# Kernel optimization log

Measured on AMD Instinct MI355X. Metric: run time of the kernel, lower is better.

Reference implementation:

```python
import jax, jax.numpy as jnp
import numpy as np

N, NFEAT, NHID, NCLASS, NLAYERS = 8192, 512, 128, 40, 3
NEG = -9e15

def _sparse_adj(key, n, density=0.002):
    u = jax.random.uniform(key, (n, n), dtype=jnp.float32)
    return jnp.where(u < density, u / density, 0.0)

def setup_inputs() -> dict:
    key = jax.random.key(0)
    ks = jax.random.split(key, 12)
    return {
        "x": jax.random.normal(ks[0], (N, NFEAT), dtype=jnp.float32),
        "adj1": _sparse_adj(ks[1], N),
        "adj2": _sparse_adj(ks[2], N),
        "adj_att": _sparse_adj(ks[3], N),
        "fc1_w": jax.random.normal(ks[4], (NLAYERS, NHID, NFEAT), dtype=jnp.float32) * (1.0 / np.sqrt(NFEAT)),
        "fc1_b": jnp.zeros((NLAYERS, NHID), jnp.float32),
        "Q_w": jax.random.normal(ks[5], (NLAYERS - 1, NHID, NHID), dtype=jnp.float32) * (1.0 / np.sqrt(NHID)),
        "Q_b": jnp.zeros((NLAYERS - 1, NHID), jnp.float32),
        "K_w": jax.random.normal(ks[6], (NLAYERS - 1, NHID, NHID), dtype=jnp.float32) * (1.0 / np.sqrt(NHID)),
        "K_b": jnp.zeros((NLAYERS - 1, NHID), jnp.float32),
        "hop_select": jnp.ones((NLAYERS,), jnp.float32),
        "w": jnp.ones((NLAYERS - 1, 2), jnp.float32),
        "clf_w": jax.random.normal(ks[7], (NCLASS, NHID * NLAYERS), dtype=jnp.float32) * (1.0 / np.sqrt(NHID * NLAYERS)),
        "clf_b": jnp.zeros((NCLASS,), jnp.float32),
    }

def _l2_normalize(x, eps=1e-12):
    # F.normalize(x, p=2, dim=1)
    n = jnp.sqrt(jnp.sum(x * x, axis=1, keepdims=True))
    return x / jnp.maximum(n, eps)

def reference(x, adj1, adj2, adj_att, fc1_w, fc1_b, Q_w, Q_b, K_w, K_b,
              hop_select, w, clf_w, clf_b):
    adj_list = [None, adj1, adj2]
    mask = jax.nn.softmax(hop_select)  # hop selection weights, shape [nlayers]
    outs = []
    for i in range(NLAYERS):
        tmp = x @ fc1_w[i].T + fc1_b[i]  # [N, nhid]
        if adj_list[i] is not None:
            adj = adj_list[i]
            W_att = jax.nn.softmax(w[i - 1])  # [2]
            tmp_att = adj_att @ tmp           # [N, nhid]
            # GCN1: linear then propagate with adj_att (act='None')
            Q = adj_att @ (tmp_att @ Q_w[i - 1].T + Q_b[i - 1])
            K = adj_att @ (tmp_att @ K_w[i - 1].T + K_b[i - 1])
            scores = Q @ K.T                  # [N, N]
            scores = jnp.where(adj > 0, scores, NEG)
            attention = jax.nn.softmax(scores, axis=-1) * W_att[0] + adj * W_att[1]
            tmp = attention @ tmp             # [N, nhid]
        tmp = _l2_normalize(tmp)
        outs.append(mask[i] * tmp)
    final = jnp.concatenate(outs, axis=1)     # [N, nhid*nlayers]
    out = jax.nn.relu(final) @ clf_w.T + clf_b  # dropout is identity in eval
    return jax.nn.log_softmax(out, axis=1)
```

## Files before the change

kernel.cpp:

```cpp
#include <hip/hip_runtime.h>
#include <hip/hip_bf16.h>

#define NN     8192
#define NFEAT  512
#define NHID   128
#define NCLASS 40
#define NLAY   3
#define CAPA   128
#define FSZ    ((size_t)NN * NHID)

typedef float f32x4 __attribute__((ext_vector_type(4)));

__global__ __launch_bounds__(256, 4) void k_d1(
    const float* __restrict__ x, const float* __restrict__ fc1w, const float* __restrict__ fc1b,
    const float* __restrict__ adjA, const float* __restrict__ hop, const float* __restrict__ w,
    float* __restrict__ tmps, float* __restrict__ f_mask, float* __restrict__ f_watt,
    float* __restrict__ colsum, float* __restrict__ rowsumA,
    int* __restrict__ cntsA, int* __restrict__ colsA, float* __restrict__ valsA)
{
    __shared__ float smem[3200];
    const int bx = blockIdx.x, tid = threadIdx.x;

    if (bx < 384) {
        float* As = smem;
        float* Bs = smem + 1088;
        const int tx = tid & 15, ty = tid >> 4;
        const int bm = (bx & 127) * 64;
        const int layer = bx >> 7;
        const int bn = layer * 128;
        float acc[4][8] = {};

        const int rA = tid >> 2, cA = (tid & 3) * 4;
        for (int kt = 0; kt < NFEAT; kt += 16) {
            f32x4 va = *reinterpret_cast<const f32x4*>(&x[(size_t)(bm + rA) * NFEAT + kt + cA]);
            As[(cA + 0) * 68 + rA] = va[0];
            As[(cA + 1) * 68 + rA] = va[1];
            As[(cA + 2) * 68 + rA] = va[2];
            As[(cA + 3) * 68 + rA] = va[3];
            #pragma unroll
            for (int it = 0; it < 2; ++it) {
                int L = tid + it * 256;
                int r = L >> 2, c4 = (L & 3) * 4;
                f32x4 vb = *reinterpret_cast<const f32x4*>(&fc1w[(size_t)(bn + r) * NFEAT + kt + c4]);
                Bs[(c4 + 0) * 132 + r] = vb[0];
                Bs[(c4 + 1) * 132 + r] = vb[1];
                Bs[(c4 + 2) * 132 + r] = vb[2];
                Bs[(c4 + 3) * 132 + r] = vb[3];
            }
            __syncthreads();
            #pragma unroll
            for (int kk = 0; kk < 16; ++kk) {
                f32x4 ra  = *reinterpret_cast<const f32x4*>(&As[kk * 68 + ty * 4]);
                f32x4 rb0 = *reinterpret_cast<const f32x4*>(&Bs[kk * 132 + tx * 4]);
                f32x4 rb1 = *reinterpret_cast<const f32x4*>(&Bs[kk * 132 + tx * 4 + 64]);
                #pragma unroll
                for (int i = 0; i < 4; ++i) {
                    #pragma unroll
                    for (int j = 0; j < 4; ++j) {
                        acc[i][j]     = fmaf(ra[i], rb0[j], acc[i][j]);
                        acc[i][j + 4] = fmaf(ra[i], rb1[j], acc[i][j + 4]);
                    }
                }
            }
            __syncthreads();
        }
        const float* bofs = fc1b + bn;
        #pragma unroll
        for (int i = 0; i < 4; ++i) {
            int m = bm + ty * 4 + i;
            #pragma unroll
            for (int j = 0; j < 8; ++j) {
                int lc = (j < 4) ? (tx * 4 + j) : (64 + tx * 4 + (j - 4));
                tmps[(size_t)layer * FSZ + (size_t)m * NHID + lc] = acc[i][j] + bofs[lc];
            }
        }
    } else if (bx < 384 + NN) {
        const int row = bx - 384;
        int* s_lcnt = (int*)smem;
        float* s_lsum = smem + 1;
        if (tid == 0) { *s_lcnt = 0; *s_lsum = 0.f; }
        __syncthreads();
        const f32x4* arow = reinterpret_cast<const f32x4*>(adjA + (size_t)row * NN);
        int* rc = colsA + (size_t)row * CAPA;
        float* rv = valsA + (size_t)row * CAPA;

        f32x4 v[8];
        #pragma unroll
        for (int i = 0; i < 8; ++i) v[i] = arow[tid + (i << 8)];

        float ls = 0.f;
        #pragma unroll
        for (int i = 0; i < 8; ++i) {
            const int c4 = tid + (i << 8);
            #pragma unroll
            for (int k = 0; k < 4; ++k) {
                if (v[i][k] > 0.f) {
                    int p = atomicAdd(s_lcnt, 1);
                    if (p < CAPA) { rc[p] = c4 * 4 + k; rv[p] = v[i][k]; }
                    ls += v[i][k];
                }
            }
        }
        if (ls != 0.f) atomicAdd(s_lsum, ls);
        __syncthreads();
        if (tid == 0) {
            int n = *s_lcnt;
            cntsA[row] = n < CAPA ? n : CAPA;
            rowsumA[row] = *s_lsum;
        }
    } else {
        colsum[tid] = 0.f;
        if (tid == 0) {
            float m = fmaxf(fmaxf(hop[0], hop[1]), hop[2]);
            float e0 = expf(hop[0] - m), e1 = expf(hop[1] - m), e2 = expf(hop[2] - m);
            float s = e0 + e1 + e2;
            f_mask[0] = e0 / s; f_mask[1] = e1 / s; f_mask[2] = e2 / s;
            for (int l = 0; l < 2; ++l) {
                float a = w[2 * l], b = w[2 * l + 1];
                float mm = fmaxf(a, b);
                float ea = expf(a - mm), eb = expf(b - mm);
                float ss = ea + eb;
                f_watt[2 * l] = ea / ss; f_watt[2 * l + 1] = eb / ss;
            }
        }
    }
}

__global__ __launch_bounds__(256, 4) void k_d2(
    const int* __restrict__ cntsA, const int* __restrict__ colsA, const float* __restrict__ valsA,
    const float* __restrict__ tmps, float* __restrict__ tmp_att, float* __restrict__ colsum,
    const float* __restrict__ adj1,
    int* __restrict__ cnts12, int* __restrict__ cols12, float* __restrict__ vals12)
{
    __shared__ int sc[CAPA];
    __shared__ float sv[CAPA];
    __shared__ int s_lcnt;
    const int bx = blockIdx.x, t = threadIdx.x;

    if (bx < NN) {
        const int row = bx;
        const int n = cntsA[row];
        for (int p = t; p < n; p += 256) { sc[p] = colsA[(size_t)row * CAPA + p]; sv[p] = valsA[(size_t)row * CAPA + p]; }
        __syncthreads();
        const int h = t >> 7, col = t & 127;
        const float* X = tmps + (size_t)(h + 1) * FSZ;
        float a0 = 0.f, a1 = 0.f, a2 = 0.f, a3 = 0.f;
        int p = 0;
        for (; p + 4 <= n; p += 4) {
            a0 = fmaf(sv[p],     X[(size_t)sc[p]     * NHID + col], a0);
            a1 = fmaf(sv[p + 1], X[(size_t)sc[p + 1] * NHID + col], a1);
            a2 = fmaf(sv[p + 2], X[(size_t)sc[p + 2] * NHID + col], a2);
            a3 = fmaf(sv[p + 3], X[(size_t)sc[p + 3] * NHID + col], a3);
        }
        for (; p < n; ++p) a0 = fmaf(sv[p], X[(size_t)sc[p] * NHID + col], a0);
        tmp_att[(size_t)h * FSZ + (size_t)row * NHID + col] = (a0 + a1) + (a2 + a3);
    } else if (bx < NN + 64) {
        const int c = bx - NN;
        const int h = t >> 7, col = t & 127;
        const float* X = tmps + (size_t)(h + 1) * FSZ + (size_t)c * 128 * NHID;
        float a = 0.f;
        for (int r = 0; r < 128; ++r) a += X[(size_t)r * NHID + col];
        atomicAdd(&colsum[h * NHID + col], a);
    } else {
        const int row = bx - NN - 64;
        if (t == 0) s_lcnt = 0;
        __syncthreads();
        const f32x4* arow = reinterpret_cast<const f32x4*>(adj1 + (size_t)row * NN);
        int* rc = cols12 + (size_t)row * CAPA;
        float* rv = vals12 + (size_t)row * CAPA;

        f32x4 v[8];
        #pragma unroll
        for (int i = 0; i < 8; ++i) v[i] = arow[t + (i << 8)];

        #pragma unroll
        for (int i = 0; i < 8; ++i) {
            const int c4 = t + (i << 8);
            #pragma unroll
            for (int k = 0; k < 4; ++k) {
                if (v[i][k] > 0.f) {
                    int p = atomicAdd(&s_lcnt, 1);
                    if (p < CAPA) { rc[p] = c4 * 4 + k; rv[p] = v[i][k]; }
                }
            }
        }
        __syncthreads();
        if (t == 0) cnts12[row] = s_lcnt < CAPA ? s_lcnt : CAPA;
    }
}

__global__ __launch_bounds__(256, 4) void k_d3(
    const int* __restrict__ cntsA, const int* __restrict__ colsA, const float* __restrict__ valsA,
    const float* __restrict__ tmp_att, const float* __restrict__ Qw, const float* __restrict__ Kw,
    const float* __restrict__ Qb, const float* __restrict__ Kb,
    const float* __restrict__ rowsumA, float* __restrict__ QKm,
    const float* __restrict__ adj2,
    int* __restrict__ cnts12, int* __restrict__ cols12, float* __restrict__ vals12)
{
    __shared__ float AsT[8192];
    const int b = blockIdx.x, tid = threadIdx.x;

    if (b < 256) {
        const int bm = (b & 127) * 64, Lz = b >> 7;
        const float* X = tmp_att + (size_t)Lz * FSZ;
        {
            const int lrow = tid >> 2, coff = (tid & 3) * 32;
            const int row = bm + lrow;
            f32x4 acc[8] = {};
            const int n = cntsA[row];
            const int* rc = colsA + (size_t)row * CAPA;
            const float* rv = valsA + (size_t)row * CAPA;
            for (int p = 0; p < n; ++p) {
                int c = rc[p];
                float v = rv[p];
                const f32x4* src = reinterpret_cast<const f32x4*>(X + (size_t)c * NHID + coff);
                #pragma unroll
                for (int j = 0; j < 8; ++j) {
                    f32x4 s = src[j];
                    acc[j][0] = fmaf(v, s[0], acc[j][0]);
                    acc[j][1] = fmaf(v, s[1], acc[j][1]);
                    acc[j][2] = fmaf(v, s[2], acc[j][2]);
                    acc[j][3] = fmaf(v, s[3], acc[j][3]);
                }
            }
            #pragma unroll
            for (int j = 0; j < 8; ++j)
                #pragma unroll
                for (int q = 0; q < 4; ++q)
                    AsT[(coff + j * 4 + q) * 64 + lrow] = acc[j][q];
        }
        __syncthreads();

        const int tx = tid & 15, ty = tid >> 4;
        float rs[4];
        #pragma unroll
        for (int i = 0; i < 4; ++i) rs[i] = rowsumA[bm + ty * 4 + i];
        float* C = QKm + (size_t)Lz * NN * 256;

        #pragma unroll
        for (int ch = 0; ch < 4; ++ch) {
            const int bn = ch * 64;
            const float* Bp; const float* bp; int bc;
            if (bn < 128) { Bp = Qw + (size_t)Lz * NHID * NHID; bp = Qb + (size_t)Lz * NHID; bc = bn; }
            else          { Bp = Kw + (size_t)Lz * NHID * NHID; bp = Kb + (size_t)Lz * NHID; bc = bn - 128; }
            float acc[4][4] = {};
            for (int k4 = 0; k4 < NHID; k4 += 4) {
                f32x4 wv[4];
                #pragma unroll
                for (int j = 0; j < 4; ++j)
                    wv[j] = *reinterpret_cast<const f32x4*>(&Bp[(size_t)(bc + tx * 4 + j) * NHID + k4]);
                #pragma unroll
                for (int q = 0; q < 4; ++q) {
                    f32x4 ra = *reinterpret_cast<const f32x4*>(&AsT[(k4 + q) * 64 + ty * 4]);
                    #pragma unroll
                    for (int i = 0; i < 4; ++i)
                        #pragma unroll
                        for (int j = 0; j < 4; ++j)
                            acc[i][j] = fmaf(ra[i], wv[j][q], acc[i][j]);
                }
            }
            #pragma unroll
            for (int i = 0; i < 4; ++i) {
                int m = bm + ty * 4 + i;
                #pragma unroll
                for (int j = 0; j < 4; ++j) {
                    int nc = bn + tx * 4 + j;
                    C[(size_t)m * 256 + nc] = acc[i][j] + rs[i] * bp[bc + tx * 4 + j];
                }
            }
        }
    } else {
        const int row = b - 256;
        int* s_lcnt = (int*)AsT;
        if (tid == 0) *s_lcnt = 0;
        __syncthreads();
        const f32x4* arow = reinterpret_cast<const f32x4*>(adj2 + (size_t)row * NN);
        int* rc = cols12 + (size_t)(NN + row) * CAPA;
        float* rv = vals12 + (size_t)(NN + row) * CAPA;

        f32x4 v[8];
        #pragma unroll
        for (int i = 0; i < 8; ++i) v[i] = arow[tid + (i << 8)];

        #pragma unroll
        for (int i = 0; i < 8; ++i) {
            const int c4 = tid + (i << 8);
            #pragma unroll
            for (int k = 0; k < 4; ++k) {
                if (v[i][k] > 0.f) {
                    int p = atomicAdd(s_lcnt, 1);
                    if (p < CAPA) { rc[p] = c4 * 4 + k; rv[p] = v[i][k]; }
                }
            }
        }
        __syncthreads();
        if (tid == 0) cnts12[NN + row] = *s_lcnt < CAPA ? *s_lcnt : CAPA;
    }
}

__global__ __launch_bounds__(256) void k_attn_clf(
    const int* __restrict__ cnts12, const int* __restrict__ cols12, const float* __restrict__ vals12,
    const float* __restrict__ QKm, const float* __restrict__ tmps,
    const float* __restrict__ colsum, const float* __restrict__ watt,
    const float* __restrict__ mask, const float* __restrict__ Wc, const float* __restrict__ bc,
    float* __restrict__ out)
{
    const int row = blockIdx.x, t = threadIdx.x;
    const int h = t >> 7, ht = t & 127;
    __shared__ int cols[2][CAPA];
    __shared__ float avals[2][CAPA];
    __shared__ float svals[2][CAPA];
    __shared__ __align__(16) float qrow[2][NHID];
    __shared__ float ws[4];
    __shared__ float ws0[2];
    __shared__ float fin[NHID * NLAY];
    __shared__ float cpart[2][64];

    const float* QK = QKm + (size_t)h * NN * 256;
    const float* T = tmps + (size_t)(h + 1) * FSZ;
    const int n = cnts12[h * NN + row];
    const int* rc = cols12 + (size_t)(h * NN + row) * CAPA;
    const float* rv = vals12 + (size_t)(h * NN + row) * CAPA;

    for (int p = ht; p < n; p += 128) { cols[h][p] = rc[p]; avals[h][p] = rv[p]; }
    if (ht < 32) *reinterpret_cast<f32x4*>(&qrow[h][ht * 4]) =
        *reinterpret_cast<const f32x4*>(QK + (size_t)row * 256 + ht * 4);
    __syncthreads();

    const float W0 = watt[h * 2], W1 = watt[h * 2 + 1];

    if (n > 0) {
        int g = ht >> 5, sl = ht & 31;
        f32x4 qv = *reinterpret_cast<const f32x4*>(&qrow[h][sl * 4]);
        for (int p = g; p < n; p += 4) {
            f32x4 kv = *reinterpret_cast<const f32x4*>(QK + (size_t)cols[h][p] * 256 + 128 + sl * 4);
            float s = qv[0] * kv[0] + qv[1] * kv[1] + qv[2] * kv[2] + qv[3] * kv[3];
            #pragma unroll
            for (int m = 16; m; m >>= 1) s += __shfl_xor(s, m);
            if (sl == 0) svals[h][p] = s;
        }
    }
    __syncthreads();

    if (n > 0 && ht < 64) {
        float mx = -3.0e38f;
        for (int p = ht; p < n; p += 64) mx = fmaxf(mx, svals[h][p]);
        #pragma unroll
        for (int m = 32; m; m >>= 1) mx = fmaxf(mx, __shfl_xor(mx, m));
        float ss = 0.f;
        for (int p = ht; p < n; p += 64) ss += expf(svals[h][p] - mx);
        #pragma unroll
        for (int m = 32; m; m >>= 1) ss += __shfl_xor(ss, m);
        float inv = 1.0f / ss;
        for (int p = ht; p < n; p += 64) avals[h][p] = expf(svals[h][p] - mx) * inv * W0 + avals[h][p] * W1;
    }
    __syncthreads();

    float acc = 0.f;
    if (n > 0) {
        float a1 = 0.f;
        int p = 0;
        for (; p + 2 <= n; p += 2) {
            acc = fmaf(avals[h][p],     T[(size_t)cols[h][p]     * NHID + ht], acc);
            a1  = fmaf(avals[h][p + 1], T[(size_t)cols[h][p + 1] * NHID + ht], a1);
        }
        if (p < n) acc = fmaf(avals[h][p], T[(size_t)cols[h][p] * NHID + ht], acc);
        acc += a1;
    } else {
        acc = W0 * (1.0f / (float)NN) * colsum[h * NHID + ht];
    }

    float s2 = acc * acc;
    #pragma unroll
    for (int m = 32; m; m >>= 1) s2 += __shfl_xor(s2, m);
    if ((t & 63) == 0) ws[t >> 6] = s2;

    float v0 = 0.f;
    if (t < 128) {
        v0 = tmps[(size_t)row * NHID + t];
        float s0 = v0 * v0;
        #pragma unroll
        for (int m = 32; m; m >>= 1) s0 += __shfl_xor(s0, m);
        if ((t & 63) == 0) ws0[t >> 6] = s0;
    }
    __syncthreads();

    {
        float d = fmaxf(sqrtf(ws[h * 2] + ws[h * 2 + 1]), 1e-12f);
        fin[(h + 1) * NHID + ht] = fmaxf(mask[h + 1] * acc / d, 0.f);
        if (t < 128) {
            float d0 = fmaxf(sqrtf(ws0[0] + ws0[1]), 1e-12f);
            fin[t] = fmaxf(mask[0] * v0 / d0, 0.f);
        }
    }
    __syncthreads();

    const int wv = t >> 6, lane = t & 63;
    if (wv < 2 && lane < NCLASS) {
        const float* wrow = Wc + (size_t)lane * (NHID * NLAY) + wv * 192;
        const float* fi = fin + wv * 192;
        float a0 = 0.f, a1 = 0.f, a2 = 0.f, a3 = 0.f;
        #pragma unroll 4
        for (int k = 0; k < 192; k += 4) {
            a0 = fmaf(fi[k],     wrow[k],     a0);
            a1 = fmaf(fi[k + 1], wrow[k + 1], a1);
            a2 = fmaf(fi[k + 2], wrow[k + 2], a2);
            a3 = fmaf(fi[k + 3], wrow[k + 3], a3);
        }
        cpart[wv][lane] = (a0 + a1) + (a2 + a3);
    }
    __syncthreads();

    if (t < 64) {
        float logit = (t < NCLASS) ? (cpart[0][t] + cpart[1][t] + bc[t]) : -3.0e38f;
        float mx = logit;
        #pragma unroll
        for (int m = 32; m; m >>= 1) mx = fmaxf(mx, __shfl_xor(mx, m));
        float e = (t < NCLASS) ? expf(logit - mx) : 0.f;
        float ssum = e;
        #pragma unroll
        for (int m = 32; m; m >>= 1) ssum += __shfl_xor(ssum, m);
        if (t < NCLASS) out[(size_t)row * NCLASS + t] = logit - mx - logf(ssum);
    }
}

extern "C" void kernel_launch(void* const* d_in, const int* in_sizes, int n_in,
                              void* d_out, int out_size, void* d_ws, size_t ws_size,
                              hipStream_t stream) {
    const float* x       = (const float*)d_in[0];
    const float* adj1    = (const float*)d_in[1];
    const float* adj2    = (const float*)d_in[2];
    const float* adj_att = (const float*)d_in[3];
    const float* fc1_w   = (const float*)d_in[4];
    const float* fc1_b   = (const float*)d_in[5];
    const float* Q_w     = (const float*)d_in[6];
    const float* Q_b     = (const float*)d_in[7];
    const float* K_w     = (const float*)d_in[8];
    const float* K_b     = (const float*)d_in[9];
    const float* hop     = (const float*)d_in[10];
    const float* w       = (const float*)d_in[11];
    const float* clf_w   = (const float*)d_in[12];
    const float* clf_b   = (const float*)d_in[13];

    float* W = (float*)d_ws;
    float* f_mask   = W;
    float* f_watt   = W + 4;
    float* f_colsum = W + 8;
    float* rowsumA  = W + 264;
    float* tmps     = W + 264 + NN;
    float* tmp_att  = tmps + 3 * FSZ;
    float* QKm      = tmp_att + 2 * FSZ;
    float* csr_valsA = QKm + 4 * FSZ;
    float* csr_vals12 = csr_valsA + FSZ;
    int*   csr_colsA = (int*)(csr_vals12 + 2 * FSZ);
    int*   csr_cols12 = csr_colsA + FSZ;
    int*   csr_cntA  = csr_cols12 + 2 * FSZ;
    int*   csr_cnt12 = csr_cntA + NN;

    size_t need = (size_t)((char*)(csr_cnt12 + 2 * NN) - (char*)d_ws);
    if (ws_size < need) return;

    k_d1<<<384 + NN + 1, 256, 0, stream>>>(
        x, fc1_w, fc1_b, adj_att, hop, w,
        tmps, f_mask, f_watt, f_colsum, rowsumA, csr_cntA, csr_colsA, csr_valsA);

    k_d2<<<NN + 64 + NN, 256, 0, stream>>>(
        csr_cntA, csr_colsA, csr_valsA, tmps, tmp_att, f_colsum,
        adj1, csr_cnt12, csr_cols12, csr_vals12);

    k_d3<<<256 + NN, 256, 0, stream>>>(
        csr_cntA, csr_colsA, csr_valsA, tmp_att, Q_w, K_w, Q_b, K_b, rowsumA, QKm,
        adj2, csr_cnt12, csr_cols12, csr_vals12);

    k_attn_clf<<<NN, 256, 0, stream>>>(
        csr_cnt12, csr_cols12, csr_vals12, QKm, tmps, f_colsum, f_watt, f_mask,
        clf_w, clf_b, (float*)d_out);
}
```

Measured before the change: 366.1 us.

## Reorganize kernel stages: split fc1 and adjacency scans, use nontemporal loads, smaller QK tiles

Splits the fused setup kernel into a separate fc1 GEMM kernel and an adj_att scan kernel. Both adj1 and adj2 scans now run in one kernel alongside the tmp_att SpMM. The QK projection becomes its own kernel with 32-row tiles over 512 blocks instead of 64-row tiles over 256 blocks, giving more parallelism. Adjacency row scans use a strided loop with nontemporal loads in place of eight preloaded vectors, to cut register pressure and keep the streamed adjacency out of cache. The cost is one extra kernel launch and less overlap between the GEMM and the scans.

```diff
diff --git a/kernel.cpp b/kernel.cpp
--- a/kernel.cpp
+++ b/kernel.cpp
@@ -2,6 +2,7 @@
 #include <hip/hip_bf16.h>
 
 #define NN     8192
+#define NF4    2048
 #define NFEAT  512
 #define NHID   128
 #define NCLASS 40
@@ -11,104 +12,17 @@
 
 typedef float f32x4 __attribute__((ext_vector_type(4)));
 
-__global__ __launch_bounds__(256, 4) void k_d1(
+__global__ __launch_bounds__(256, 4) void k_fc1(
     const float* __restrict__ x, const float* __restrict__ fc1w, const float* __restrict__ fc1b,
-    const float* __restrict__ adjA, const float* __restrict__ hop, const float* __restrict__ w,
+    const float* __restrict__ hop, const float* __restrict__ w,
     float* __restrict__ tmps, float* __restrict__ f_mask, float* __restrict__ f_watt,
-    float* __restrict__ colsum, float* __restrict__ rowsumA,
-    int* __restrict__ cntsA, int* __restrict__ colsA, float* __restrict__ valsA)
+    float* __restrict__ colsum)
 {
     __shared__ float smem[3200];
-    const int bx = blockIdx.x, tid = threadIdx.x;
-
-    if (bx < 384) {
-        float* As = smem;
-        float* Bs = smem + 1088;
-        const int tx = tid & 15, ty = tid >> 4;
-        const int bm = (bx & 127) * 64;
-        const int layer = bx >> 7;
-        const int bn = layer * 128;
-        float acc[4][8] = {};
-
-        const int rA = tid >> 2, cA = (tid & 3) * 4;
-        for (int kt = 0; kt < NFEAT; kt += 16) {
-            f32x4 va = *reinterpret_cast<const f32x4*>(&x[(size_t)(bm + rA) * NFEAT + kt + cA]);
-            As[(cA + 0) * 68 + rA] = va[0];
-            As[(cA + 1) * 68 + rA] = va[1];
-            As[(cA + 2) * 68 + rA] = va[2];
-            As[(cA + 3) * 68 + rA] = va[3];
-            #pragma unroll
-            for (int it = 0; it < 2; ++it) {
-                int L = tid + it * 256;
-                int r = L >> 2, c4 = (L & 3) * 4;
-                f32x4 vb = *reinterpret_cast<const f32x4*>(&fc1w[(size_t)(bn + r) * NFEAT + kt + c4]);
-                Bs[(c4 + 0) * 132 + r] = vb[0];
-                Bs[(c4 + 1) * 132 + r] = vb[1];
-                Bs[(c4 + 2) * 132 + r] = vb[2];
-                Bs[(c4 + 3) * 132 + r] = vb[3];
-            }
-            __syncthreads();
-            #pragma unroll
-            for (int kk = 0; kk < 16; ++kk) {
-                f32x4 ra  = *reinterpret_cast<const f32x4*>(&As[kk * 68 + ty * 4]);
-                f32x4 rb0 = *reinterpret_cast<const f32x4*>(&Bs[kk * 132 + tx * 4]);
-                f32x4 rb1 = *reinterpret_cast<const f32x4*>(&Bs[kk * 132 + tx * 4 + 64]);
-                #pragma unroll
-                for (int i = 0; i < 4; ++i) {
-                    #pragma unroll
-                    for (int j = 0; j < 4; ++j) {
-                        acc[i][j]     = fmaf(ra[i], rb0[j], acc[i][j]);
-                        acc[i][j + 4] = fmaf(ra[i], rb1[j], acc[i][j + 4]);
-                    }
-                }
-            }
-            __syncthreads();
-        }
-        const float* bofs = fc1b + bn;
-        #pragma unroll
-        for (int i = 0; i < 4; ++i) {
-            int m = bm + ty * 4 + i;
-            #pragma unroll
-            for (int j = 0; j < 8; ++j) {
-                int lc = (j < 4) ? (tx * 4 + j) : (64 + tx * 4 + (j - 4));
-                tmps[(size_t)layer * FSZ + (size_t)m * NHID + lc] = acc[i][j] + bofs[lc];
-            }
-        }
-    } else if (bx < 384 + NN) {
-        const int row = bx - 384;
-        int* s_lcnt = (int*)smem;
-        float* s_lsum = smem + 1;
-        if (tid == 0) { *s_lcnt = 0; *s_lsum = 0.f; }
-        __syncthreads();
-        const f32x4* arow = reinterpret_cast<const f32x4*>(adjA + (size_t)row * NN);
-        int* rc = colsA + (size_t)row * CAPA;
-        float* rv = valsA + (size_t)row * CAPA;
-
-        f32x4 v[8];
-        #pragma unroll
-        for (int i = 0; i < 8; ++i) v[i] = arow[tid + (i << 8)];
-
-        float ls = 0.f;
-        #pragma unroll
-        for (int i = 0; i < 8; ++i) {
-            const int c4 = tid + (i << 8);
-            #pragma unroll
-            for (int k = 0; k < 4; ++k) {
-                if (v[i][k] > 0.f) {
-                    int p = atomicAdd(s_lcnt, 1);
-                    if (p < CAPA) { rc[p] = c4 * 4 + k; rv[p] = v[i][k]; }
-                    ls += v[i][k];
-                }
-            }
-        }
-        if (ls != 0.f) atomicAdd(s_lsum, ls);
-        __syncthreads();
-        if (tid == 0) {
-            int n = *s_lcnt;
-            cntsA[row] = n < CAPA ? n : CAPA;
-            rowsumA[row] = *s_lsum;
-        }
-    } else {
+    const int bx = blockIdx.x, layer = blockIdx.y, tid = threadIdx.x;
+
+    if (bx == 128) {
+        if (layer != 0) return;
         colsum[tid] = 0.f;
         if (tid == 0) {
             float m = fmaxf(fmaxf(hop[0], hop[1]), hop[2]);
@@ -123,13 +37,99 @@
                 f_watt[2 * l] = ea / ss; f_watt[2 * l + 1] = eb / ss;
             }
         }
-    }
-}
-
-__global__ __launch_bounds__(256, 4) void k_d2(
+        return;
+    }
+
+    float* As = smem;
+    float* Bs = smem + 1088;
+    const int tx = tid & 15, ty = tid >> 4;
+    const int bm = bx * 64;
+    const int bn = layer * 128;
+    float acc[4][8] = {};
+
+    const int rA = tid >> 2, cA = (tid & 3) * 4;
+    for (int kt = 0; kt < NFEAT; kt += 16) {
+        f32x4 va = *reinterpret_cast<const f32x4*>(&x[(size_t)(bm + rA) * NFEAT + kt + cA]);
+        As[(cA + 0) * 68 + rA] = va[0];
+        As[(cA + 1) * 68 + rA] = va[1];
+        As[(cA + 2) * 68 + rA] = va[2];
+        As[(cA + 3) * 68 + rA] = va[3];
+        #pragma unroll
+        for (int it = 0; it < 2; ++it) {
+            int L = tid + it * 256;
+            int r = L >> 2, c4 = (L & 3) * 4;
+            f32x4 vb = *reinterpret_cast<const f32x4*>(&fc1w[(size_t)(bn + r) * NFEAT + kt + c4]);
+            Bs[(c4 + 0) * 132 + r] = vb[0];
+            Bs[(c4 + 1) * 132 + r] = vb[1];
+            Bs[(c4 + 2) * 132 + r] = vb[2];
+            Bs[(c4 + 3) * 132 + r] = vb[3];
+        }
+        __syncthreads();
+        #pragma unroll
+        for (int kk = 0; kk < 16; ++kk) {
+            f32x4 ra  = *reinterpret_cast<const f32x4*>(&As[kk * 68 + ty * 4]);
+            f32x4 rb0 = *reinterpret_cast<const f32x4*>(&Bs[kk * 132 + tx * 4]);
+            f32x4 rb1 = *reinterpret_cast<const f32x4*>(&Bs[kk * 132 + tx * 4 + 64]);
+            #pragma unroll
+            for (int i = 0; i < 4; ++i) {
+                #pragma unroll
+                for (int j = 0; j < 4; ++j) {
+                    acc[i][j]     = fmaf(ra[i], rb0[j], acc[i][j]);
+                    acc[i][j + 4] = fmaf(ra[i], rb1[j], acc[i][j + 4]);
+                }
+            }
+        }
+        __syncthreads();
+    }
+    const float* bofs = fc1b + bn;
+    #pragma unroll
+    for (int i = 0; i < 4; ++i) {
+        int m = bm + ty * 4 + i;
+        #pragma unroll
+        for (int j = 0; j < 8; ++j) {
+            int lc = (j < 4) ? (tx * 4 + j) : (64 + tx * 4 + (j - 4));
+            tmps[(size_t)layer * FSZ + (size_t)m * NHID + lc] = acc[i][j] + bofs[lc];
+        }
+    }
+}
+
+__global__ __launch_bounds__(256) void k_scanA(
+    const float* __restrict__ adjA,
+    int* __restrict__ cntsA, int* __restrict__ colsA, float* __restrict__ valsA,
+    float* __restrict__ rowsumA)
+{
+    const int row = blockIdx.x, tid = threadIdx.x;
+    __shared__ int s_lcnt;
+    __shared__ float s_lsum;
+    if (tid == 0) { s_lcnt = 0; s_lsum = 0.f; }
+    __syncthreads();
+    const f32x4* arow = reinterpret_cast<const f32x4*>(adjA + (size_t)row * NN);
+    int* rc = colsA + (size_t)row * CAPA;
+    float* rv = valsA + (size_t)row * CAPA;
+    float ls = 0.f;
+    for (int c4 = tid; c4 < NF4; c4 += 256) {
+        f32x4 v = __builtin_nontemporal_load(&arow[c4]);
+        #pragma unroll
+        for (int k = 0; k < 4; ++k) {
+            if (v[k] > 0.f) {
+                int p = atomicAdd(&s_lcnt, 1);
+                if (p < CAPA) { rc[p] = c4 * 4 + k; rv[p] = v[k]; }
+                ls += v[k];
+            }
+        }
+    }
+    if (ls != 0.f) atomicAdd(&s_lsum, ls);
+    __syncthreads();
+    if (tid == 0) {
+        cntsA[row] = s_lcnt < CAPA ? s_lcnt : CAPA;
+        rowsumA[row] = s_lsum;
+    }
+}
+
+__global__ __launch_bounds__(256) void k_d3(
+    const float* __restrict__ adj1, const float* __restrict__ adj2,
     const int* __restrict__ cntsA, const int* __restrict__ colsA, const float* __restrict__ valsA,
     const float* __restrict__ tmps, float* __restrict__ tmp_att, float* __restrict__ colsum,
-    const float* __restrict__ adj1,
     int* __restrict__ cnts12, int* __restrict__ cols12, float* __restrict__ vals12)
 {
     __shared__ int sc[CAPA];
@@ -137,8 +137,28 @@
     __shared__ int s_lcnt;
     const int bx = blockIdx.x, t = threadIdx.x;
 
-    if (bx < NN) {
-        const int row = bx;
+    if (bx < 2 * NN) {
+        const int mat = bx >> 13, row = bx & (NN - 1);
+        const float* adj = mat ? adj2 : adj1;
+        if (t == 0) s_lcnt = 0;
+        __syncthreads();
+        const f32x4* arow = reinterpret_cast<const f32x4*>(adj + (size_t)row * NN);
+        int* rc = cols12 + (size_t)(mat * NN + row) * CAPA;
+        float* rv = vals12 + (size_t)(mat * NN + row) * CAPA;
+        for (int c4 = t; c4 < NF4; c4 += 256) {
+            f32x4 v = __builtin_nontemporal_load(&arow[c4]);
+            #pragma unroll
+            for (int k = 0; k < 4; ++k) {
+                if (v[k] > 0.f) {
+                    int p = atomicAdd(&s_lcnt, 1);
+                    if (p < CAPA) { rc[p] = c4 * 4 + k; rv[p] = v[k]; }
+                }
+            }
+        }
+        __syncthreads();
+        if (t == 0) cnts12[mat * NN + row] = s_lcnt < CAPA ? s_lcnt : CAPA;
+    } else if (bx < 3 * NN) {
+        const int row = bx - 2 * NN;
         const int n = cntsA[row];
         for (int p = t; p < n; p += 256) { sc[p] = colsA[(size_t)row * CAPA + p]; sv[p] = valsA[(size_t)row * CAPA + p]; }
         __syncthreads();
@@ -154,147 +174,92 @@
         }
         for (; p < n; ++p) a0 = fmaf(sv[p], X[(size_t)sc[p] * NHID + col], a0);
         tmp_att[(size_t)h * FSZ + (size_t)row * NHID + col] = (a0 + a1) + (a2 + a3);
-    } else if (bx < NN + 64) {
-        const int c = bx - NN;
+    } else {
+        const int c = bx - 3 * NN;
         const int h = t >> 7, col = t & 127;
         const float* X = tmps + (size_t)(h + 1) * FSZ + (size_t)c * 128 * NHID;
         float a = 0.f;
         for (int r = 0; r < 128; ++r) a += X[(size_t)r * NHID + col];
         atomicAdd(&colsum[h * NHID + col], a);
-    } else {
-        const int row = bx - NN - 64;
-        if (t == 0) s_lcnt = 0;
-        __syncthreads();
-        const f32x4* arow = reinterpret_cast<const f32x4*>(adj1 + (size_t)row * NN);
-        int* rc = cols12 + (size_t)row * CAPA;
-        float* rv = vals12 + (size_t)row * CAPA;
-
-        f32x4 v[8];
-        #pragma unroll
-        for (int i = 0; i < 8; ++i) v[i] = arow[t + (i << 8)];
-
-        #pragma unroll
-        for (int i = 0; i < 8; ++i) {
-            const int c4 = t + (i << 8);
-            #pragma unroll
-            for (int k = 0; k < 4; ++k) {
-                if (v[i][k] > 0.f) {
-                    int p = atomicAdd(&s_lcnt, 1);
-                    if (p < CAPA) { rc[p] = c4 * 4 + k; rv[p] = v[i][k]; }
-                }
-            }
-        }
-        __syncthreads();
-        if (t == 0) cnts12[row] = s_lcnt < CAPA ? s_lcnt : CAPA;
-    }
-}
-
-__global__ __launch_bounds__(256, 4) void k_d3(
+    }
+}
+
+__global__ __launch_bounds__(256, 4) void k_t2qkm(
     const int* __restrict__ cntsA, const int* __restrict__ colsA, const float* __restrict__ valsA,
     const float* __restrict__ tmp_att, const float* __restrict__ Qw, const float* __restrict__ Kw,
     const float* __restrict__ Qb, const float* __restrict__ Kb,
-    const float* __restrict__ rowsumA, float* __restrict__ QKm,
-    const float* __restrict__ adj2,
-    int* __restrict__ cnts12, int* __restrict__ cols12, float* __restrict__ vals12)
+    const float* __restrict__ rowsumA, float* __restrict__ QKm)
 {
-    __shared__ float AsT[8192];
-    const int b = blockIdx.x, tid = threadIdx.x;
-
-    if (b < 256) {
-        const int bm = (b & 127) * 64, Lz = b >> 7;
-        const float* X = tmp_att + (size_t)Lz * FSZ;
-        {
-            const int lrow = tid >> 2, coff = (tid & 3) * 32;
-            const int row = bm + lrow;
-            f32x4 acc[8] = {};
-            const int n = cntsA[row];
-            const int* rc = colsA + (size_t)row * CAPA;
-            const float* rv = valsA + (size_t)row * CAPA;
-            for (int p = 0; p < n; ++p) {
-                int c = rc[p];
-                float v = rv[p];
-                const f32x4* src = reinterpret_cast<const f32x4*>(X + (size_t)c * NHID + coff);
-                #pragma unroll
-                for (int j = 0; j < 8; ++j) {
-                    f32x4 s = src[j];
-                    acc[j][0] = fmaf(v, s[0], acc[j][0]);
-                    acc[j][1] = fmaf(v, s[1], acc[j][1]);
-                    acc[j][2] = fmaf(v, s[2], acc[j][2]);
-                    acc[j][3] = fmaf(v, s[3], acc[j][3]);
-                }
-            }
-            #pragma unroll
-            for (int j = 0; j < 8; ++j)
-                #pragma unroll
-                for (int q = 0; q < 4; ++q)
-                    AsT[(coff + j * 4 + q) * 64 + lrow] = acc[j][q];
-        }
-        __syncthreads();
-
-        const int tx = tid & 15, ty = tid >> 4;
-        float rs[4];
-        #pragma unroll
-        for (int i = 0; i < 4; ++i) rs[i] = rowsumA[bm + ty * 4 + i];
-        float* C = QKm + (size_t)Lz * NN * 256;
-
-        #pragma unroll
-        for (int ch = 0; ch < 4; ++ch) {
-            const int bn = ch * 64;
-            const float* Bp; const float* bp; int bc;
-            if (bn < 128) { Bp = Qw + (size_t)Lz * NHID * NHID; bp = Qb + (size_t)Lz * NHID; bc = bn; }
-            else          { Bp = Kw + (size_t)Lz * NHID * NHID; bp = Kb + (size_t)Lz * NHID; bc = bn - 128; }
-            float acc[4][4] = {};
-            for (int k4 = 0; k4 < NHID; k4 += 4) {
-                f32x4 wv[4];
-                #pragma unroll
-                for (int j = 0; j < 4; ++j)
-                    wv[j] = *reinterpret_cast<const f32x4*>(&Bp[(size_t)(bc + tx * 4 + j) * NHID + k4]);
-                #pragma unroll
-                for (int q = 0; q < 4; ++q) {
-                    f32x4 ra = *reinterpret_cast<const f32x4*>(&AsT[(k4 + q) * 64 + ty * 4]);
-                    #pragma unroll
-                    for (int i = 0; i < 4; ++i)
-                        #pragma unroll
-                        for (int j = 0; j < 4; ++j)
-                            acc[i][j] = fmaf(ra[i], wv[j][q], acc[i][j]);
-                }
-            }
-            #pragma unroll
-            for (int i = 0; i < 4; ++i) {
-                int m = bm + ty * 4 + i;
+    __shared__ float AsT[128 * 33];
+    const int tid = threadIdx.x;
+    const int bm = (blockIdx.x & 255) * 32, Lz = blockIdx.x >> 8;
+    const float* X = tmp_att + (size_t)Lz * FSZ;
+
+    {
+        const int lrow = tid >> 3, coff = (tid & 7) * 16;
+        const int row = bm + lrow;
+        f32x4 acc[4] = {};
+        const int n = cntsA[row];
+        const int* rc = colsA + (size_t)row * CAPA;
+        const float* rv = valsA + (size_t)row * CAPA;
+        for (int p = 0; p < n; ++p) {
+            int c = rc[p];
+            float v = rv[p];
+            const f32x4* src = reinterpret_cast<const f32x4*>(X + (size_t)c * NHID + coff);
+            #pragma unroll
+            for (int j = 0; j < 4; ++j) {
+                f32x4 s = src[j];
+                acc[j][0] = fmaf(v, s[0], acc[j][0]);
+                acc[j][1] = fmaf(v, s[1], acc[j][1]);
+                acc[j][2] = fmaf(v, s[2], acc[j][2]);
+                acc[j][3] = fmaf(v, s[3], acc[j][3]);
+            }
+        }
+        #pragma unroll
+        for (int j = 0; j < 4; ++j)
+            #pragma unroll
+            for (int q = 0; q < 4; ++q)
+                AsT[(coff + j * 4 + q) * 33 + lrow] = acc[j][q];
+    }
+    __syncthreads();
+
+    const int tx = tid & 15, ty = tid >> 4;
+    float rs0 = rowsumA[bm + ty * 2], rs1 = rowsumA[bm + ty * 2 + 1];
+    float* C = QKm + (size_t)Lz * NN * 256;
+
+    #pragma unroll
+    for (int ch = 0; ch < 4; ++ch) {
+        const int bn = ch * 64;
+        const float* Bp; const float* bp; int bc;
+        if (bn < 128) { Bp = Qw + (size_t)Lz * NHID * NHID; bp = Qb + (size_t)Lz * NHID; bc = bn; }
+        else          { Bp = Kw + (size_t)Lz * NHID * NHID; bp = Kb + (size_t)Lz * NHID; bc = bn - 128; }
+        float acc[2][4] = {};
+        for (int k4 = 0; k4 < NHID; k4 += 4) {
+            f32x4 wv[4];
+            #pragma unroll
+            for (int j = 0; j < 4; ++j)
+                wv[j] = *reinterpret_cast<const f32x4*>(&Bp[(size_t)(bc + tx * 4 + j) * NHID + k4]);
+            #pragma unroll
+            for (int q = 0; q < 4; ++q) {
+                float ra0 = AsT[(k4 + q) * 33 + ty * 2];
+                float ra1 = AsT[(k4 + q) * 33 + ty * 2 + 1];
                 #pragma unroll
                 for (int j = 0; j < 4; ++j) {
-                    int nc = bn + tx * 4 + j;
-                    C[(size_t)m * 256 + nc] = acc[i][j] + rs[i] * bp[bc + tx * 4 + j];
+                    acc[0][j] = fmaf(ra0, wv[j][q], acc[0][j]);
+                    acc[1][j] = fmaf(ra1, wv[j][q], acc[1][j]);
                 }
             }
         }
-    } else {
-        const int row = b - 256;
-        int* s_lcnt = (int*)AsT;
-        if (tid == 0) *s_lcnt = 0;
-        __syncthreads();
-        const f32x4* arow = reinterpret_cast<const f32x4*>(adj2 + (size_t)row * NN);
-        int* rc = cols12 + (size_t)(NN + row) * CAPA;
-        float* rv = vals12 + (size_t)(NN + row) * CAPA;
-
-        f32x4 v[8];
-        #pragma unroll
-        for (int i = 0; i < 8; ++i) v[i] = arow[tid + (i << 8)];
-
-        #pragma unroll
-        for (int i = 0; i < 8; ++i) {
-            const int c4 = tid + (i << 8);
-            #pragma unroll
-            for (int k = 0; k < 4; ++k) {
-                if (v[i][k] > 0.f) {
-                    int p = atomicAdd(s_lcnt, 1);
-                    if (p < CAPA) { rc[p] = c4 * 4 + k; rv[p] = v[i][k]; }
-                }
-            }
-        }
-        __syncthreads();
-        if (tid == 0) cnts12[NN + row] = *s_lcnt < CAPA ? *s_lcnt : CAPA;
+        #pragma unroll
+        for (int i = 0; i < 2; ++i) {
+            int m = bm + ty * 2 + i;
+            float rs = i ? rs1 : rs0;
+            #pragma unroll
+            for (int j = 0; j < 4; ++j) {
+                int nc = bn + tx * 4 + j;
+                C[(size_t)m * 256 + nc] = acc[i][j] + rs * bp[bc + tx * 4 + j];
+            }
+        }
     }
 }
 
@@ -460,17 +425,17 @@
     size_t need = (size_t)((char*)(csr_cnt12 + 2 * NN) - (char*)d_ws);
     if (ws_size < need) return;
 
-    k_d1<<<384 + NN + 1, 256, 0, stream>>>(
-        x, fc1_w, fc1_b, adj_att, hop, w,
-        tmps, f_mask, f_watt, f_colsum, rowsumA, csr_cntA, csr_colsA, csr_valsA);
-
-    k_d2<<<NN + 64 + NN, 256, 0, stream>>>(
-        csr_cntA, csr_colsA, csr_valsA, tmps, tmp_att, f_colsum,
-        adj1, csr_cnt12, csr_cols12, csr_vals12);
-
-    k_d3<<<256 + NN, 256, 0, stream>>>(
-        csr_cntA, csr_colsA, csr_valsA, tmp_att, Q_w, K_w, Q_b, K_b, rowsumA, QKm,
-        adj2, csr_cnt12, csr_cols12, csr_vals12);
+    k_fc1<<<dim3(129, 3), 256, 0, stream>>>(
+        x, fc1_w, fc1_b, hop, w, tmps, f_mask, f_watt, f_colsum);
+
+    k_scanA<<<NN, 256, 0, stream>>>(adj_att, csr_cntA, csr_colsA, csr_valsA, rowsumA);
+
+    k_d3<<<3 * NN + 64, 256, 0, stream>>>(
+        adj1, adj2, csr_cntA, csr_colsA, csr_valsA, tmps, tmp_att, f_colsum,
+        csr_cnt12, csr_cols12, csr_vals12);
+
+    k_t2qkm<<<512, 256, 0, stream>>>(
+        csr_cntA, csr_colsA, csr_valsA, tmp_att, Q_w, K_w, Q_b, K_b, rowsumA, QKm);
 
     k_attn_clf<<<NN, 256, 0, stream>>>(
         csr_cnt12, csr_cols12, csr_vals12, QKm, tmps, f_colsum, f_watt, f_mask,
```

Result: slower. 433.3 us (+18.3%).
